# Kernel optimization log

Measured on AMD Instinct MI355X. Metric: run time of the kernel, lower is better.

The kernel has to match this reference:

```python
import jax, jax.numpy as jnp
import numpy as np

N_QUBITS = 8   # out_channels = number of wires
KERNEL = 4     # kernel_size
N_LAYERS = 4
STRIDE = 1
PAD = 1


def _rx(t):
    c = jnp.cos(t * 0.5).astype(jnp.complex64)
    s = jnp.sin(t * 0.5).astype(jnp.complex64)
    return jnp.stack([jnp.stack([c, -1j * s]), jnp.stack([-1j * s, c])])


def _ry(t):
    c = jnp.cos(t * 0.5).astype(jnp.complex64)
    s = jnp.sin(t * 0.5).astype(jnp.complex64)
    return jnp.stack([jnp.stack([c, -s]), jnp.stack([s, c])])


def _rz(t):
    e = jnp.exp(-0.5j * t.astype(jnp.complex64))
    z = jnp.zeros((), jnp.complex64)
    return jnp.stack([jnp.stack([e, z]), jnp.stack([z, jnp.conj(e)])])


def _ap1(state, U, w):
    # apply 2x2 gate U on qubit axis w of state shaped (2,)*N_QUBITS
    s = jnp.moveaxis(state, w, -1)
    s = s @ U.T
    return jnp.moveaxis(s, -1, w)


def _cnot(state, c, t):
    s0 = jax.lax.index_in_dim(state, 0, axis=c, keepdims=True)
    s1 = jax.lax.index_in_dim(state, 1, axis=c, keepdims=True)
    return jnp.concatenate([s0, jnp.flip(s1, axis=t)], axis=c)


def _ansatz(state, wl):  # wl: (N_QUBITS, 3) angles for layer i (custom_layers)
    for j in range(N_QUBITS):
        c, t = (j, j + 1) if j < N_QUBITS - 1 else (0, j)
        state = _ap1(state, _rx(wl[j, 0]), j)
        state = _cnot(state, c, t)
        state = _ap1(state, _ry(wl[j, 1]), j)
        state = _cnot(state, c, t)
        state = _ap1(state, _rz(wl[j, 2]), j)
    return state


def _circuit(inputs, weights):
    # inputs: (KERNEL,) patch; weights: (N_LAYERS+1, N_QUBITS, 3)
    state = jnp.zeros((2,) * N_QUBITS, jnp.complex64).at[(0,) * N_QUBITS].set(1.0)
    state = _ansatz(state, weights[0])
    for i in range(1, N_LAYERS + 1):
        w = 0
        for _ in range(N_QUBITS // KERNEL):  # 'parallel': re-upload data each layer
            for k in range(KERNEL):
                state = _ap1(state, _ry(inputs[k]), w + k)
            w += KERNEL
        state = _ansatz(state, weights[i])
    probs = state.real ** 2 + state.imag ** 2
    sign = jnp.array([1.0, -1.0], jnp.float32)
    z = [jnp.sum(probs, axis=tuple(a for a in range(N_QUBITS) if a != j)) @ sign
         for j in range(N_QUBITS)]
    return jnp.stack(z)  # (N_QUBITS,) <PauliZ_j>


def _forward(vector, weights):
    bs, ch, l = vector.shape
    if ch > 1:
        vector = vector.mean(axis=-2).reshape(bs, 1, l)
    v = jnp.pad(vector, ((0, 0), (0, 0), (PAD, PAD)))
    l_out = (l + 2 * PAD - KERNEL) // STRIDE + 1
    idx = jnp.arange(l_out)[:, None] * STRIDE + jnp.arange(KERNEL)  # (l_out, K)
    patches = v[:, 0, :][:, idx].reshape(bs * l_out, KERNEL)
    q = jax.vmap(_circuit, in_axes=(0, None))(patches, weights)  # (bs*l_out, N_QUBITS)
    out = q.reshape(bs, l_out, N_QUBITS).transpose(0, 2, 1)  # (bs, C, l_out)
    out = jax.nn.relu(out)
    return jnp.max(out, axis=-1, keepdims=True)  # (bs, C, 1)


def setup_inputs() -> dict:
    key = jax.random.key(0)
    k1, k2 = jax.random.split(key)
    vector = jax.random.normal(k1, (8, 1, 512), jnp.float32)
    # flax nn.initializers.normal() default stddev = 0.01
    weights = jax.random.normal(k2, (N_LAYERS + 1, N_QUBITS, 3), jnp.float32) * 0.01
    return {"vector": vector, "weights": weights}


def reference(vector, weights):
    return _forward(vector, weights)
```

## Files before the change

kernel.cpp:

```cpp
#include <hip/hip_runtime.h>

#define NQ 8
#define KK 4
#define LIN 512
#define LOUT 511
#define BATCH 8
#define NCIRC (BATCH * LOUT)
#define NBLOCKS (NCIRC / 8)

#define ENC0 0xC0000000u
__device__ unsigned g_acc[BATCH * NQ];
__device__ unsigned g_cnt;

template<int M> __device__ __forceinline__ float lx(float v) {
    if constexpr (M == 1)
        return __builtin_bit_cast(float, __builtin_amdgcn_update_dpp(
            0, __builtin_bit_cast(int, v), 0xB1, 0xF, 0xF, true));
    else if constexpr (M == 2)
        return __builtin_bit_cast(float, __builtin_amdgcn_update_dpp(
            0, __builtin_bit_cast(int, v), 0x4E, 0xF, 0xF, true));
    else if constexpr (M == 3)
        return __builtin_bit_cast(float, __builtin_amdgcn_update_dpp(
            0, __builtin_bit_cast(int, v), 0x1B, 0xF, 0xF, true));
    else if constexpr (M == 8)
        return __builtin_bit_cast(float, __builtin_amdgcn_update_dpp(
            0, __builtin_bit_cast(int, v), 0x128, 0xF, 0xF, true));
    else
        return __builtin_bit_cast(float, __builtin_amdgcn_ds_swizzle(
            __builtin_bit_cast(int, v), (M << 10) | 0x1F));
}

template<int LB>
__device__ __forceinline__ void rx_lane(float (&sr)[8], float (&si)[8], float c, float s) {
    constexpr int M = 1 << LB;
    #pragma unroll
    for (int r = 0; r < 8; ++r) {
        float orr = lx<M>(sr[r]), oii = lx<M>(si[r]);
        float nr = c * sr[r] + s * oii;
        float ni = c * si[r] - s * orr;
        sr[r] = nr; si[r] = ni;
    }
}

template<int LB>
__device__ __forceinline__ void ry_lane(float (&sr)[8], float (&si)[8], float c, float s, int lane) {
    constexpr int M = 1 << LB;
    const float sg = ((lane >> LB) & 1) ? s : -s;
    #pragma unroll
    for (int r = 0; r < 8; ++r) {
        float orr = lx<M>(sr[r]), oii = lx<M>(si[r]);
        sr[r] = c * sr[r] + sg * orr;
        si[r] = c * si[r] + sg * oii;
    }
}

template<int LB>
__device__ __forceinline__ void rz_lane(float (&sr)[8], float (&si)[8], float c, float s, int lane) {
    const float t = ((lane >> LB) & 1) ? -s : s;
    #pragma unroll
    for (int r = 0; r < 8; ++r) {
        float nr = c * sr[r] + t * si[r];
        float ni = c * si[r] - t * sr[r];
        sr[r] = nr; si[r] = ni;
    }
}

template<int RB>
__device__ __forceinline__ void rx_reg(float (&sr)[8], float (&si)[8], float c, float s) {
    constexpr int m = 1 << RB;
    #pragma unroll
    for (int r = 0; r < 8; ++r) {
        if ((r & m) == 0) {
            const int a = r, b = r | m;
            float ar = sr[a], ai = si[a], br = sr[b], bi = si[b];
            sr[a] = c*ar + s*bi;  si[a] = c*ai - s*br;
            sr[b] = c*br + s*ai;  si[b] = c*bi - s*ar;
        }
    }
}

template<int RB>
__device__ __forceinline__ void ry_reg(float (&sr)[8], float (&si)[8], float c, float s) {
    constexpr int m = 1 << RB;
    #pragma unroll
    for (int r = 0; r < 8; ++r) {
        if ((r & m) == 0) {
            const int a = r, b = r | m;
            float ar = sr[a], ai = si[a], br = sr[b], bi = si[b];
            sr[a] = c*ar - s*br;  si[a] = c*ai - s*bi;
            sr[b] = s*ar + c*br;  si[b] = s*ai + c*bi;
        }
    }
}

template<int RB>
__device__ __forceinline__ void rz_reg(float (&sr)[8], float (&si)[8], float c, float s) {
    #pragma unroll
    for (int r = 0; r < 8; ++r) {
        const float t = ((r >> RB) & 1) ? -s : s;
        float nr = c * sr[r] + t * si[r];
        float ni = c * si[r] - t * sr[r];
        sr[r] = nr; si[r] = ni;
    }
}

template<int LBc, int LBt>
__device__ __forceinline__ void fry_ll(float (&sr)[8], float (&si)[8], float c, float s, int lane) {
    constexpr int M = (1 << LBc) | (1 << LBt);
    const float sg = ((lane >> LBc) & 1) ? s : -s;
    #pragma unroll
    for (int r = 0; r < 8; ++r) {
        float orr = lx<M>(sr[r]), oii = lx<M>(si[r]);
        sr[r] = c * sr[r] + sg * orr;
        si[r] = c * si[r] + sg * oii;
    }
}

template<int LBc, int RBt>
__device__ __forceinline__ void fry_lr(float (&sr)[8], float (&si)[8], float c, float s, int lane) {
    constexpr int M = 1 << LBc;
    constexpr int mt = 1 << RBt;
    const float sg = ((lane >> LBc) & 1) ? s : -s;
    float pr[8], pi[8];
    #pragma unroll
    for (int r = 0; r < 8; ++r) { pr[r] = lx<M>(sr[r ^ mt]); pi[r] = lx<M>(si[r ^ mt]); }
    #pragma unroll
    for (int r = 0; r < 8; ++r) { sr[r] = c*sr[r] + sg*pr[r]; si[r] = c*si[r] + sg*pi[r]; }
}

template<int RBc, int RBt>
__device__ __forceinline__ void fry_rr(float (&sr)[8], float (&si)[8], float c, float s) {
    constexpr int mm = (1 << RBc) | (1 << RBt);
    float nr[8], ni[8];
    #pragma unroll
    for (int r = 0; r < 8; ++r) {
        const float sg = ((r >> RBc) & 1) ? s : -s;
        nr[r] = c*sr[r] + sg*sr[r ^ mm];
        ni[r] = c*si[r] + sg*si[r ^ mm];
    }
    #pragma unroll
    for (int r = 0; r < 8; ++r) { sr[r] = nr[r]; si[r] = ni[r]; }
}

__device__ __forceinline__ void cry_q7(float (&sr)[8], float (&si)[8], float c, float s, int lane) {
    const float se = ((lane >> 4) & 1) ? -s : s;
    #pragma unroll
    for (int p = 0; p < 4; ++p) {
        const int a = 2*p, b = 2*p + 1;
        float ar = sr[a], ai = si[a], br = sr[b], bi = si[b];
        sr[a] = c*ar - se*br;  si[a] = c*ai - se*bi;
        sr[b] = se*ar + c*br;  si[b] = se*ai + c*bi;
    }
}

template<bool LAST>
__device__ __forceinline__ void ansatz8(float (&sr)[8], float (&si)[8],
                                        const float (&tc)[24], const float (&ts)[24], int lane) {
    rx_lane<4>(sr, si, tc[0], ts[0]);
    fry_ll<4,3>(sr, si, tc[1], ts[1], lane);
    if (!LAST) rz_lane<4>(sr, si, tc[2], ts[2], lane);
    rx_lane<3>(sr, si, tc[3], ts[3]);
    fry_ll<3,2>(sr, si, tc[4], ts[4], lane);
    if (!LAST) rz_lane<3>(sr, si, tc[5], ts[5], lane);
    rx_lane<2>(sr, si, tc[6], ts[6]);
    fry_ll<2,1>(sr, si, tc[7], ts[7], lane);
    if (!LAST) rz_lane<2>(sr, si, tc[8], ts[8], lane);
    rx_lane<1>(sr, si, tc[9], ts[9]);
    fry_ll<1,0>(sr, si, tc[10], ts[10], lane);
    if (!LAST) rz_lane<1>(sr, si, tc[11], ts[11], lane);
    rx_lane<0>(sr, si, tc[12], ts[12]);
    fry_lr<0,2>(sr, si, tc[13], ts[13], lane);
    if (!LAST) rz_lane<0>(sr, si, tc[14], ts[14], lane);
    rx_reg<2>(sr, si, tc[15], ts[15]);
    fry_rr<2,1>(sr, si, tc[16], ts[16]);
    if (!LAST) rz_reg<2>(sr, si, tc[17], ts[17]);
    rx_reg<1>(sr, si, tc[18], ts[18]);
    fry_rr<1,0>(sr, si, tc[19], ts[19]);
    if (!LAST) rz_reg<1>(sr, si, tc[20], ts[20]);
    rx_reg<0>(sr, si, tc[21], ts[21]);
    cry_q7(sr, si, tc[22], ts[22], lane);
    if (!LAST) rz_reg<0>(sr, si, tc[23], ts[23]);
}

__device__ __forceinline__ void reup8(float (&sr)[8], float (&si)[8],
                                      const float (&xc)[4], const float (&xs)[4], int lane) {
    ry_lane<4>(sr, si, xc[0], xs[0], lane);  ry_lane<0>(sr, si, xc[0], xs[0], lane);
    ry_lane<3>(sr, si, xc[1], xs[1], lane);  ry_reg<2>(sr, si, xc[1], xs[1]);
    ry_lane<2>(sr, si, xc[2], xs[2], lane);  ry_reg<1>(sr, si, xc[2], xs[2]);
    ry_lane<1>(sr, si, xc[3], xs[3], lane);  ry_reg<0>(sr, si, xc[3], xs[3]);
}

template<int ST>
__device__ __forceinline__ void bstage8(float (&z)[8], int lane) {
    constexpr int M = 1 << ST;
    #pragma unroll
    for (int q = 0; q < 8; ++q) {
        float o = lx<M>(z[q]);
        if (q < 5 && (4 - q) == ST)
            z[q] = ((lane >> ST) & 1) ? (o - z[q]) : (z[q] - o);
        else
            z[q] += o;
    }
}

__device__ __forceinline__ void layer_trig(const float* __restrict__ wl,
                                           float (&tc)[24], float (&ts)[24], int lane) {
    float a = (lane < 24) ? 0.5f * wl[lane] : 0.0f;
    float s, c;
    __sincosf(a, &s, &c);
    #pragma unroll
    for (int i = 0; i < 24; ++i) {
        tc[i] = __builtin_bit_cast(float,
            __builtin_amdgcn_readlane(__builtin_bit_cast(int, c), i));
        ts[i] = __builtin_bit_cast(float,
            __builtin_amdgcn_readlane(__builtin_bit_cast(int, s), i));
    }
}

__global__ __launch_bounds__(256) void quanv_kernel(const float* __restrict__ vec,
                                                    const float* __restrict__ wts,
                                                    float* __restrict__ out) {
    const int tid = threadIdx.x;
    const int lane = tid & 63;
    const int pos = tid & 31;
    const int circ = blockIdx.x * 8 + (tid >> 5);
    const int b = circ / LOUT;
    const int op = circ - b * LOUT;

    float xc[4], xs[4];
    #pragma unroll
    for (int k = 0; k < KK; ++k) {
        int idx = op - 1 + k;
        int ic = idx < 0 ? 0 : (idx > LIN - 1 ? LIN - 1 : idx);
        float xv = vec[b * LIN + ic];
        xv = (idx == ic) ? xv : 0.0f;
        float a = 0.5f * xv;
        xs[k] = __sinf(a); xc[k] = __cosf(a);
    }

    float sr[8] = {0,0,0,0,0,0,0,0};
    float si[8] = {0,0,0,0,0,0,0,0};
    if (pos == 0) sr[0] = 1.0f;

    float tc[24], ts[24];
    layer_trig(wts, tc, ts, lane);
    ansatz8<false>(sr, si, tc, ts, lane);

    #pragma unroll 1
    for (int L = 1; L <= 3; ++L) {
        layer_trig(wts + L * 24, tc, ts, lane);
        reup8(sr, si, xc, xs, lane);
        ansatz8<false>(sr, si, tc, ts, lane);
    }
    layer_trig(wts + 4 * 24, tc, ts, lane);
    reup8(sr, si, xc, xs, lane);
    ansatz8<true>(sr, si, tc, ts, lane);

    float p[8];
    #pragma unroll
    for (int r = 0; r < 8; ++r) p[r] = sr[r]*sr[r] + si[r]*si[r];
    float pl = 0.f, z5 = 0.f, z6 = 0.f, z7 = 0.f;
    #pragma unroll
    for (int r = 0; r < 8; ++r) {
        pl += p[r];
        z5 += ((r >> 2) & 1) ? -p[r] : p[r];
        z6 += ((r >> 1) & 1) ? -p[r] : p[r];
        z7 += ( r       & 1) ? -p[r] : p[r];
    }
    float z[8];
    z[0] = pl; z[1] = pl; z[2] = pl; z[3] = pl; z[4] = pl;
    z[5] = z5; z[6] = z6; z[7] = z7;

    bstage8<0>(z, lane); bstage8<1>(z, lane); bstage8<2>(z, lane);
    bstage8<3>(z, lane); bstage8<4>(z, lane);

    __shared__ float zsh[8][NQ];
    __shared__ int bsh[8];
    __shared__ int lastFlag;
    const int g = tid >> 5;
    if (pos == 0) {
        bsh[g] = b;
        #pragma unroll
        for (int q = 0; q < NQ; ++q) zsh[g][q] = fmaxf(z[q], 0.0f);
    }
    __syncthreads();
    if (tid < 64) {
        const int gg = tid >> 3, q = tid & 7;
        const bool leader = (gg == 0) || (bsh[gg] != bsh[gg - 1]);
        if (leader) {
            float m = zsh[gg][q];
            for (int g2 = gg + 1; g2 < 8 && bsh[g2] == bsh[gg]; ++g2)
                m = fmaxf(m, zsh[g2][q]);
            atomicMax(&g_acc[bsh[gg] * NQ + q], __float_as_uint(m) + ENC0);
        }
    }
    __syncthreads();

    if (tid == 0) {
        __threadfence();
        unsigned old = atomicAdd(&g_cnt, 1u);
        lastFlag = (old == NBLOCKS - 1);
    }
    __syncthreads();
    if (lastFlag && tid < BATCH * NQ) {
        unsigned e = atomicMax(&g_acc[tid], 0u);
        out[tid] = __uint_as_float(e - ENC0);
        g_acc[tid] = ENC0;
        if (tid == 0) g_cnt = 0u;
    }
}

extern "C" void kernel_launch(void* const* d_in, const int* in_sizes, int n_in,
                              void* d_out, int out_size, void* d_ws, size_t ws_size,
                              hipStream_t stream) {
    const float* vec = (const float*)d_in[0];
    const float* wts = (const float*)d_in[1];
    float* out = (float*)d_out;

    hipLaunchKernelGGL(quanv_kernel, dim3(NBLOCKS), dim3(256), 0, stream, vec, wts, out);
}
```

Measured before the change: 77.59 us.

## Pack complex state into float2 vectors and precompute gate trig in LDS

Stores each complex amplitude as a two-float vector so gate updates can map to packed FP32 multiply-add instructions. Gate cosines and sines for all layers are computed once per block into shared memory, replacing the per-layer sincos plus readlane broadcasts. All five layers now run in one non-unrolled loop with a runtime last-layer flag, which adds branches and LDS reads of the gate table. New DPP cases are added to the lane-exchange helper, though the ansatz does not appear to use those masks.

```diff
diff --git a/kernel.cpp b/kernel.cpp
--- a/kernel.cpp
+++ b/kernel.cpp
@@ -12,182 +12,192 @@
 __device__ unsigned g_acc[BATCH * NQ];
 __device__ unsigned g_cnt;
 
+typedef float v2f __attribute__((ext_vector_type(2)));
+
+template<int CTRL> __device__ __forceinline__ float dpp1(float v) {
+    return __builtin_bit_cast(float, __builtin_amdgcn_update_dpp(
+        0, __builtin_bit_cast(int, v), CTRL, 0xF, 0xF, true));
+}
 template<int M> __device__ __forceinline__ float lx(float v) {
-    if constexpr (M == 1)
-        return __builtin_bit_cast(float, __builtin_amdgcn_update_dpp(
-            0, __builtin_bit_cast(int, v), 0xB1, 0xF, 0xF, true));
-    else if constexpr (M == 2)
-        return __builtin_bit_cast(float, __builtin_amdgcn_update_dpp(
-            0, __builtin_bit_cast(int, v), 0x4E, 0xF, 0xF, true));
-    else if constexpr (M == 3)
-        return __builtin_bit_cast(float, __builtin_amdgcn_update_dpp(
-            0, __builtin_bit_cast(int, v), 0x1B, 0xF, 0xF, true));
-    else if constexpr (M == 8)
-        return __builtin_bit_cast(float, __builtin_amdgcn_update_dpp(
-            0, __builtin_bit_cast(int, v), 0x128, 0xF, 0xF, true));
+    if constexpr (M == 1)       return dpp1<0xB1>(v);
+    else if constexpr (M == 2)  return dpp1<0x4E>(v);
+    else if constexpr (M == 3)  return dpp1<0x1B>(v);
+    else if constexpr (M == 7)  return dpp1<0x141>(v);
+    else if constexpr (M == 8)  return dpp1<0x128>(v);
+    else if constexpr (M == 15) return dpp1<0x140>(v);
+    else if constexpr (M == 4)  return lx<3>(lx<7>(v));
+    else if constexpr (M == 5)  return lx<2>(lx<7>(v));
+    else if constexpr (M == 6)  return lx<1>(lx<7>(v));
+    else if constexpr (M == 12) return lx<3>(lx<15>(v));
     else
         return __builtin_bit_cast(float, __builtin_amdgcn_ds_swizzle(
             __builtin_bit_cast(int, v), (M << 10) | 0x1F));
 }
 
 template<int LB>
-__device__ __forceinline__ void rx_lane(float (&sr)[8], float (&si)[8], float c, float s) {
+__device__ __forceinline__ void rx_lane(v2f (&st)[8], float c, float s) {
     constexpr int M = 1 << LB;
-    #pragma unroll
-    for (int r = 0; r < 8; ++r) {
-        float orr = lx<M>(sr[r]), oii = lx<M>(si[r]);
-        float nr = c * sr[r] + s * oii;
-        float ni = c * si[r] - s * orr;
-        sr[r] = nr; si[r] = ni;
+    const v2f c2 = {c, c}, sv = {s, -s};
+    #pragma unroll
+    for (int r = 0; r < 8; ++r) {
+        v2f ov = { lx<M>(st[r].y), lx<M>(st[r].x) };
+        st[r] = c2 * st[r] + sv * ov;
     }
 }
 
 template<int LB>
-__device__ __forceinline__ void ry_lane(float (&sr)[8], float (&si)[8], float c, float s, int lane) {
+__device__ __forceinline__ void ry_lane(v2f (&st)[8], float c, float s, int lane) {
     constexpr int M = 1 << LB;
     const float sg = ((lane >> LB) & 1) ? s : -s;
-    #pragma unroll
-    for (int r = 0; r < 8; ++r) {
-        float orr = lx<M>(sr[r]), oii = lx<M>(si[r]);
-        sr[r] = c * sr[r] + sg * orr;
-        si[r] = c * si[r] + sg * oii;
+    const v2f c2 = {c, c}, sg2 = {sg, sg};
+    #pragma unroll
+    for (int r = 0; r < 8; ++r) {
+        v2f ov = { lx<M>(st[r].x), lx<M>(st[r].y) };
+        st[r] = c2 * st[r] + sg2 * ov;
     }
 }
 
 template<int LB>
-__device__ __forceinline__ void rz_lane(float (&sr)[8], float (&si)[8], float c, float s, int lane) {
+__device__ __forceinline__ void rz_lane(v2f (&st)[8], float c, float s, int lane) {
     const float t = ((lane >> LB) & 1) ? -s : s;
-    #pragma unroll
-    for (int r = 0; r < 8; ++r) {
-        float nr = c * sr[r] + t * si[r];
-        float ni = c * si[r] - t * sr[r];
-        sr[r] = nr; si[r] = ni;
+    const v2f c2 = {c, c}, tv = {t, -t};
+    #pragma unroll
+    for (int r = 0; r < 8; ++r) {
+        v2f sw = { st[r].y, st[r].x };
+        st[r] = c2 * st[r] + tv * sw;
     }
 }
 
 template<int RB>
-__device__ __forceinline__ void rx_reg(float (&sr)[8], float (&si)[8], float c, float s) {
+__device__ __forceinline__ void rx_reg(v2f (&st)[8], float c, float s) {
     constexpr int m = 1 << RB;
+    const v2f c2 = {c, c}, sv = {s, -s};
     #pragma unroll
     for (int r = 0; r < 8; ++r) {
         if ((r & m) == 0) {
             const int a = r, b = r | m;
-            float ar = sr[a], ai = si[a], br = sr[b], bi = si[b];
-            sr[a] = c*ar + s*bi;  si[a] = c*ai - s*br;
-            sr[b] = c*br + s*ai;  si[b] = c*bi - s*ar;
+            v2f A = st[a], B = st[b];
+            v2f swA = { A.y, A.x }, swB = { B.y, B.x };
+            st[a] = c2 * A + sv * swB;
+            st[b] = c2 * B + sv * swA;
         }
     }
 }
 
 template<int RB>
-__device__ __forceinline__ void ry_reg(float (&sr)[8], float (&si)[8], float c, float s) {
+__device__ __forceinline__ void ry_reg(v2f (&st)[8], float c, float s) {
     constexpr int m = 1 << RB;
+    const v2f c2 = {c, c}, s2 = {s, s};
     #pragma unroll
     for (int r = 0; r < 8; ++r) {
         if ((r & m) == 0) {
             const int a = r, b = r | m;
-            float ar = sr[a], ai = si[a], br = sr[b], bi = si[b];
-            sr[a] = c*ar - s*br;  si[a] = c*ai - s*bi;
-            sr[b] = s*ar + c*br;  si[b] = s*ai + c*bi;
+            v2f A = st[a], B = st[b];
+            st[a] = c2 * A - s2 * B;
+            st[b] = c2 * B + s2 * A;
         }
     }
 }
 
 template<int RB>
-__device__ __forceinline__ void rz_reg(float (&sr)[8], float (&si)[8], float c, float s) {
+__device__ __forceinline__ void rz_reg(v2f (&st)[8], float c, float s) {
+    const v2f c2 = {c, c};
     #pragma unroll
     for (int r = 0; r < 8; ++r) {
         const float t = ((r >> RB) & 1) ? -s : s;
-        float nr = c * sr[r] + t * si[r];
-        float ni = c * si[r] - t * sr[r];
-        sr[r] = nr; si[r] = ni;
+        const v2f tv = {t, -t};
+        v2f sw = { st[r].y, st[r].x };
+        st[r] = c2 * st[r] + tv * sw;
     }
 }
 
 template<int LBc, int LBt>
-__device__ __forceinline__ void fry_ll(float (&sr)[8], float (&si)[8], float c, float s, int lane) {
+__device__ __forceinline__ void fry_ll(v2f (&st)[8], float c, float s, int lane) {
     constexpr int M = (1 << LBc) | (1 << LBt);
     const float sg = ((lane >> LBc) & 1) ? s : -s;
-    #pragma unroll
-    for (int r = 0; r < 8; ++r) {
-        float orr = lx<M>(sr[r]), oii = lx<M>(si[r]);
-        sr[r] = c * sr[r] + sg * orr;
-        si[r] = c * si[r] + sg * oii;
+    const v2f c2 = {c, c}, sg2 = {sg, sg};
+    #pragma unroll
+    for (int r = 0; r < 8; ++r) {
+        v2f ov = { lx<M>(st[r].x), lx<M>(st[r].y) };
+        st[r] = c2 * st[r] + sg2 * ov;
     }
 }
 
 template<int LBc, int RBt>
-__device__ __forceinline__ void fry_lr(float (&sr)[8], float (&si)[8], float c, float s, int lane) {
+__device__ __forceinline__ void fry_lr(v2f (&st)[8], float c, float s, int lane) {
     constexpr int M = 1 << LBc;
     constexpr int mt = 1 << RBt;
     const float sg = ((lane >> LBc) & 1) ? s : -s;
-    float pr[8], pi[8];
-    #pragma unroll
-    for (int r = 0; r < 8; ++r) { pr[r] = lx<M>(sr[r ^ mt]); pi[r] = lx<M>(si[r ^ mt]); }
-    #pragma unroll
-    for (int r = 0; r < 8; ++r) { sr[r] = c*sr[r] + sg*pr[r]; si[r] = c*si[r] + sg*pi[r]; }
+    const v2f c2 = {c, c}, sg2 = {sg, sg};
+    v2f ov[8];
+    #pragma unroll
+    for (int r = 0; r < 8; ++r)
+        ov[r] = v2f{ lx<M>(st[r ^ mt].x), lx<M>(st[r ^ mt].y) };
+    #pragma unroll
+    for (int r = 0; r < 8; ++r)
+        st[r] = c2 * st[r] + sg2 * ov[r];
 }
 
 template<int RBc, int RBt>
-__device__ __forceinline__ void fry_rr(float (&sr)[8], float (&si)[8], float c, float s) {
+__device__ __forceinline__ void fry_rr(v2f (&st)[8], float c, float s) {
     constexpr int mm = (1 << RBc) | (1 << RBt);
-    float nr[8], ni[8];
+    const v2f c2 = {c, c};
+    v2f nv[8];
     #pragma unroll
     for (int r = 0; r < 8; ++r) {
         const float sg = ((r >> RBc) & 1) ? s : -s;
-        nr[r] = c*sr[r] + sg*sr[r ^ mm];
-        ni[r] = c*si[r] + sg*si[r ^ mm];
-    }
-    #pragma unroll
-    for (int r = 0; r < 8; ++r) { sr[r] = nr[r]; si[r] = ni[r]; }
-}
-
-__device__ __forceinline__ void cry_q7(float (&sr)[8], float (&si)[8], float c, float s, int lane) {
+        const v2f sg2 = {sg, sg};
+        nv[r] = c2 * st[r] + sg2 * st[r ^ mm];
+    }
+    #pragma unroll
+    for (int r = 0; r < 8; ++r) st[r] = nv[r];
+}
+
+__device__ __forceinline__ void cry_q7(v2f (&st)[8], float c, float s, int lane) {
     const float se = ((lane >> 4) & 1) ? -s : s;
+    const v2f c2 = {c, c}, se2 = {se, se};
     #pragma unroll
     for (int p = 0; p < 4; ++p) {
         const int a = 2*p, b = 2*p + 1;
-        float ar = sr[a], ai = si[a], br = sr[b], bi = si[b];
-        sr[a] = c*ar - se*br;  si[a] = c*ai - se*bi;
-        sr[b] = se*ar + c*br;  si[b] = se*ai + c*bi;
-    }
-}
-
-template<bool LAST>
-__device__ __forceinline__ void ansatz8(float (&sr)[8], float (&si)[8],
-                                        const float (&tc)[24], const float (&ts)[24], int lane) {
-    rx_lane<4>(sr, si, tc[0], ts[0]);
-    fry_ll<4,3>(sr, si, tc[1], ts[1], lane);
-    if (!LAST) rz_lane<4>(sr, si, tc[2], ts[2], lane);
-    rx_lane<3>(sr, si, tc[3], ts[3]);
-    fry_ll<3,2>(sr, si, tc[4], ts[4], lane);
-    if (!LAST) rz_lane<3>(sr, si, tc[5], ts[5], lane);
-    rx_lane<2>(sr, si, tc[6], ts[6]);
-    fry_ll<2,1>(sr, si, tc[7], ts[7], lane);
-    if (!LAST) rz_lane<2>(sr, si, tc[8], ts[8], lane);
-    rx_lane<1>(sr, si, tc[9], ts[9]);
-    fry_ll<1,0>(sr, si, tc[10], ts[10], lane);
-    if (!LAST) rz_lane<1>(sr, si, tc[11], ts[11], lane);
-    rx_lane<0>(sr, si, tc[12], ts[12]);
-    fry_lr<0,2>(sr, si, tc[13], ts[13], lane);
-    if (!LAST) rz_lane<0>(sr, si, tc[14], ts[14], lane);
-    rx_reg<2>(sr, si, tc[15], ts[15]);
-    fry_rr<2,1>(sr, si, tc[16], ts[16]);
-    if (!LAST) rz_reg<2>(sr, si, tc[17], ts[17]);
-    rx_reg<1>(sr, si, tc[18], ts[18]);
-    fry_rr<1,0>(sr, si, tc[19], ts[19]);
-    if (!LAST) rz_reg<1>(sr, si, tc[20], ts[20]);
-    rx_reg<0>(sr, si, tc[21], ts[21]);
-    cry_q7(sr, si, tc[22], ts[22], lane);
-    if (!LAST) rz_reg<0>(sr, si, tc[23], ts[23]);
-}
-
-__device__ __forceinline__ void reup8(float (&sr)[8], float (&si)[8],
+        v2f A = st[a], B = st[b];
+        st[a] = c2 * A - se2 * B;
+        st[b] = c2 * B + se2 * A;
+    }
+}
+
+__device__ __forceinline__ void ansatz8(v2f (&st)[8], const v2f (&t)[24], int lane, bool last) {
+    rx_lane<4>(st, t[0].x, t[0].y);
+    fry_ll<4,3>(st, t[1].x, t[1].y, lane);
+    if (!last) rz_lane<4>(st, t[2].x, t[2].y, lane);
+    rx_lane<3>(st, t[3].x, t[3].y);
+    fry_ll<3,2>(st, t[4].x, t[4].y, lane);
+    if (!last) rz_lane<3>(st, t[5].x, t[5].y, lane);
+    rx_lane<2>(st, t[6].x, t[6].y);
+    fry_ll<2,1>(st, t[7].x, t[7].y, lane);
+    if (!last) rz_lane<2>(st, t[8].x, t[8].y, lane);
+    rx_lane<1>(st, t[9].x, t[9].y);
+    fry_ll<1,0>(st, t[10].x, t[10].y, lane);
+    if (!last) rz_lane<1>(st, t[11].x, t[11].y, lane);
+    rx_lane<0>(st, t[12].x, t[12].y);
+    fry_lr<0,2>(st, t[13].x, t[13].y, lane);
+    if (!last) rz_lane<0>(st, t[14].x, t[14].y, lane);
+    rx_reg<2>(st, t[15].x, t[15].y);
+    fry_rr<2,1>(st, t[16].x, t[16].y);
+    if (!last) rz_reg<2>(st, t[17].x, t[17].y);
+    rx_reg<1>(st, t[18].x, t[18].y);
+    fry_rr<1,0>(st, t[19].x, t[19].y);
+    if (!last) rz_reg<1>(st, t[20].x, t[20].y);
+    rx_reg<0>(st, t[21].x, t[21].y);
+    cry_q7(st, t[22].x, t[22].y, lane);
+    if (!last) rz_reg<0>(st, t[23].x, t[23].y);
+}
+
+__device__ __forceinline__ void reup8(v2f (&st)[8],
                                       const float (&xc)[4], const float (&xs)[4], int lane) {
-    ry_lane<4>(sr, si, xc[0], xs[0], lane);  ry_lane<0>(sr, si, xc[0], xs[0], lane);
-    ry_lane<3>(sr, si, xc[1], xs[1], lane);  ry_reg<2>(sr, si, xc[1], xs[1]);
-    ry_lane<2>(sr, si, xc[2], xs[2], lane);  ry_reg<1>(sr, si, xc[2], xs[2]);
-    ry_lane<1>(sr, si, xc[3], xs[3], lane);  ry_reg<0>(sr, si, xc[3], xs[3]);
+    ry_lane<4>(st, xc[0], xs[0], lane);  ry_lane<0>(st, xc[0], xs[0], lane);
+    ry_lane<3>(st, xc[1], xs[1], lane);  ry_reg<2>(st, xc[1], xs[1]);
+    ry_lane<2>(st, xc[2], xs[2], lane);  ry_reg<1>(st, xc[2], xs[2]);
+    ry_lane<1>(st, xc[3], xs[3], lane);  ry_reg<0>(st, xc[3], xs[3]);
 }
 
 template<int ST>
@@ -203,24 +213,18 @@
     }
 }
 
-__device__ __forceinline__ void layer_trig(const float* __restrict__ wl,
-                                           float (&tc)[24], float (&ts)[24], int lane) {
-    float a = (lane < 24) ? 0.5f * wl[lane] : 0.0f;
-    float s, c;
-    __sincosf(a, &s, &c);
-    #pragma unroll
-    for (int i = 0; i < 24; ++i) {
-        tc[i] = __builtin_bit_cast(float,
-            __builtin_amdgcn_readlane(__builtin_bit_cast(int, c), i));
-        ts[i] = __builtin_bit_cast(float,
-            __builtin_amdgcn_readlane(__builtin_bit_cast(int, s), i));
-    }
-}
-
 __global__ __launch_bounds__(256) void quanv_kernel(const float* __restrict__ vec,
                                                     const float* __restrict__ wts,
                                                     float* __restrict__ out) {
+    __shared__ v2f tt2[120];
     const int tid = threadIdx.x;
+    if (tid < 120) {
+        float a = 0.5f * wts[tid];
+        float s, c;
+        __sincosf(a, &s, &c);
+        tt2[tid] = v2f{c, s};
+    }
+
     const int lane = tid & 63;
     const int pos = tid & 31;
     const int circ = blockIdx.x * 8 + (tid >> 5);
@@ -238,27 +242,25 @@
         xs[k] = __sinf(a); xc[k] = __cosf(a);
     }
 
-    float sr[8] = {0,0,0,0,0,0,0,0};
-    float si[8] = {0,0,0,0,0,0,0,0};
-    if (pos == 0) sr[0] = 1.0f;
-
-    float tc[24], ts[24];
-    layer_trig(wts, tc, ts, lane);
-    ansatz8<false>(sr, si, tc, ts, lane);
+    v2f st[8];
+    #pragma unroll
+    for (int r = 0; r < 8; ++r) st[r] = v2f{0.f, 0.f};
+    if (pos == 0) st[0] = v2f{1.f, 0.f};
+
+    __syncthreads();
 
     #pragma unroll 1
-    for (int L = 1; L <= 3; ++L) {
-        layer_trig(wts + L * 24, tc, ts, lane);
-        reup8(sr, si, xc, xs, lane);
-        ansatz8<false>(sr, si, tc, ts, lane);
-    }
-    layer_trig(wts + 4 * 24, tc, ts, lane);
-    reup8(sr, si, xc, xs, lane);
-    ansatz8<true>(sr, si, tc, ts, lane);
+    for (int L = 0; L <= 4; ++L) {
+        v2f tab[24];
+        #pragma unroll
+        for (int i = 0; i < 24; ++i) tab[i] = tt2[L * 24 + i];
+        if (L) reup8(st, xc, xs, lane);
+        ansatz8(st, tab, lane, L == 4);
+    }
 
     float p[8];
     #pragma unroll
-    for (int r = 0; r < 8; ++r) p[r] = sr[r]*sr[r] + si[r]*si[r];
+    for (int r = 0; r < 8; ++r) p[r] = st[r].x*st[r].x + st[r].y*st[r].y;
     float pl = 0.f, z5 = 0.f, z6 = 0.f, z7 = 0.f;
     #pragma unroll
     for (int r = 0; r < 8; ++r) {
```

After: 76.85 us. No clear change (-0.9%).
